# Kernel tuning notes

Measured on AMD Instinct MI355X. Metric: run time of the kernel, lower is better.

The kernel has to match this reference:

```python
import jax, jax.numpy as jnp
import numpy as np

B, T, V, E, H, L = 2, 1024, 50257, 768, 12, 12
D = E // H  # 64
FF = 4 * E
SCALE = 1.0 / (E * E)  # module divides scores by C**2 where C = embedding_dim
EPS = 1e-5


def _layernorm(x, g, b):
    m = jnp.mean(x, axis=-1, keepdims=True)
    v = jnp.mean((x - m) ** 2, axis=-1, keepdims=True)
    return (x - m) * jax.lax.rsqrt(v + EPS) * g + b


def setup_inputs() -> dict:
    key = jax.random.key(0)
    ks = jax.random.split(key, 12)
    s = 0.02
    f32 = jnp.float32
    return {
        "idx": jax.random.randint(ks[0], (B, T), 0, V),
        "tok_emb": jax.random.normal(ks[1], (V, E), f32) * s,
        "pos_emb": jax.random.normal(ks[2], (T, E), f32) * s,
        "Wk": jax.random.normal(ks[3], (L, H, E, D), f32) * s,
        "Wq": jax.random.normal(ks[4], (L, H, E, D), f32) * s,
        "Wv": jax.random.normal(ks[5], (L, H, E, D), f32) * s,
        "Wproj": jax.random.normal(ks[6], (L, E, E), f32) * s,
        "bproj": jnp.zeros((L, E), f32),
        "ln1_g": jnp.ones((L, E), f32),
        "ln1_b": jnp.zeros((L, E), f32),
        "W1": jax.random.normal(ks[7], (L, E, FF), f32) * s,
        "b1": jnp.zeros((L, FF), f32),
        "W2": jax.random.normal(ks[8], (L, FF, E), f32) * s,
        "b2": jnp.zeros((L, E), f32),
        "ln2_g": jnp.ones((L, E), f32),
        "ln2_b": jnp.zeros((L, E), f32),
        "lnf_g": jnp.ones((E,), f32),
        "lnf_b": jnp.zeros((E,), f32),
        "Wlm": jax.random.normal(ks[9], (E, V), f32) * s,
        "blm": jnp.zeros((V,), f32),
    }


def reference(idx, tok_emb, pos_emb, Wk, Wq, Wv, Wproj, bproj, ln1_g, ln1_b,
              W1, b1, W2, b2, ln2_g, ln2_b, lnf_g, lnf_b, Wlm, blm):
    x = tok_emb[idx] + pos_emb[:T]  # [B,T,E]
    causal = jnp.tril(jnp.ones((T, T), bool))

    def layer(x, p):
        wk, wq, wv, wp, bp, g1, be1, w1, bb1, w2, bb2, g2, be2 = p
        h = _layernorm(x, g1, be1)
        k = jnp.einsum('bte,hed->bhtd', h, wk)
        q = jnp.einsum('bte,hed->bhtd', h, wq)
        v = jnp.einsum('bte,hed->bhtd', h, wv)
        # faithful to source: scores = k @ q^T, scaled by 1/E^2
        scores = jnp.einsum('bhtd,bhsd->bhts', k, q) * SCALE
        scores = jnp.where(causal, scores, -jnp.inf)
        attn = jax.nn.softmax(scores, axis=-1)
        o = jnp.einsum('bhts,bhsd->bhtd', attn, v)
        o = o.transpose(0, 2, 1, 3).reshape(B, T, E)  # concat heads
        x = x + o @ wp + bp
        h2 = _layernorm(x, g2, be2)
        x = x + jax.nn.relu(h2 @ w1 + bb1) @ w2 + bb2
        return x, None

    x, _ = jax.lax.scan(layer, x, (Wk, Wq, Wv, Wproj, bproj, ln1_g, ln1_b,
                                   W1, b1, W2, b2, ln2_g, ln2_b))
    x = _layernorm(x, lnf_g, lnf_b)
    logits = x @ Wlm + blm  # [B,T,V]
    return logits
```

## Files before the change

### kernel.cpp

```cpp
#include <hip/hip_runtime.h>
#include <hip/hip_bf16.h>
#include <stdint.h>

#define B_    2
#define T_    1024
#define V_    50257
#define VPAD_ 50304
#define VPAD2_ 50432
#define E_    768
#define H_    12
#define L_    12
#define D_    64
#define FF_   3072
#define NTOK  (B_*T_)
#define SCALE_ (1.0f/((float)E_*(float)E_))

#define SWZ(r) ((((r) ^ ((r) >> 2)) & 3))

typedef float f32x4 __attribute__((ext_vector_type(4)));
typedef __bf16 bf16x8 __attribute__((ext_vector_type(8)));
typedef short short8 __attribute__((ext_vector_type(8)));

__device__ __forceinline__ float bits2f(short s) {
    unsigned u = ((unsigned)(unsigned short)s) << 16;
    float f; __builtin_memcpy(&f, &u, 4); return f;
}
__device__ __forceinline__ short f2b(float f) {
    unsigned u; __builtin_memcpy(&u, &f, 4);
    unsigned r = (u + 0x7FFFu + ((u >> 16) & 1u)) >> 16;
    return (short)r;
}

#define GLOAD16(gsrc, ldst) __builtin_amdgcn_global_load_lds( \
    (const __attribute__((address_space(1))) unsigned*)(gsrc), \
    (__attribute__((address_space(3))) unsigned*)(ldst), 16, 0, 0)

__global__ __launch_bounds__(256) void embed_kernel(
    const int* __restrict__ idx, const float* __restrict__ tok,
    const float* __restrict__ pos, float* __restrict__ x)
{
    int m = blockIdx.x, tid = threadIdx.x;
    int row = idx[m];
    int t = m & (T_-1);
    #pragma unroll
    for (int i = 0; i < 3; i++) {
        int e = tid + i*256;
        x[(size_t)m*E_ + e] = tok[(size_t)row*E_ + e] + pos[(size_t)t*E_ + e];
    }
}

__device__ __forceinline__ float block_sum256(float v, float* red) {
    #pragma unroll
    for (int off = 32; off; off >>= 1) v += __shfl_xor(v, off, 64);
    int w = threadIdx.x >> 6;
    __syncthreads();
    if ((threadIdx.x & 63) == 0) red[w] = v;
    __syncthreads();
    return red[0] + red[1] + red[2] + red[3];
}

__global__ __launch_bounds__(256) void ln_kernel(
    const float* __restrict__ x, const float* __restrict__ g,
    const float* __restrict__ bb, short* __restrict__ out)
{
    __shared__ float red[4];
    int m = blockIdx.x, tid = threadIdx.x;
    const float* xr = x + (size_t)m*E_;
    float loc[3]; float s = 0.f;
    #pragma unroll
    for (int i = 0; i < 3; i++) { loc[i] = xr[tid + i*256]; s += loc[i]; }
    s = block_sum256(s, red);
    float mean = s * (1.0f/E_);
    float vs = 0.f;
    #pragma unroll
    for (int i = 0; i < 3; i++) { float d = loc[i] - mean; vs += d*d; }
    vs = block_sum256(vs, red);
    float rstd = rsqrtf(vs * (1.0f/E_) + 1e-5f);
    #pragma unroll
    for (int i = 0; i < 3; i++) {
        int e = tid + i*256;
        out[(size_t)m*E_ + e] = f2b((loc[i] - mean) * rstd * g[e] + bb[e]);
    }
}

template<int NS>
__global__ __launch_bounds__(256) void ln_red(
    float* __restrict__ x, const float* __restrict__ pb,
    const float* __restrict__ bias,
    const float* __restrict__ g, const float* __restrict__ bb,
    short* __restrict__ out)
{
    __shared__ float red[4];
    int m = blockIdx.x, tid = threadIdx.x;
    float* xr = x + (size_t)m*E_;
    float loc[3]; float s = 0.f;
    #pragma unroll
    for (int i = 0; i < 3; i++) {
        int e = tid + i*256;
        float v = xr[e];
        if (NS > 0) {
            #pragma unroll
            for (int sp = 0; sp < NS; sp++)
                v += pb[((size_t)sp*NTOK + m)*E_ + e];
            v += bias[e];
            xr[e] = v;
        }
        loc[i] = v; s += v;
    }
    s = block_sum256(s, red);
    float mean = s * (1.0f/E_);
    float vs = 0.f;
    #pragma unroll
    for (int i = 0; i < 3; i++) { float d = loc[i] - mean; vs += d*d; }
    vs = block_sum256(vs, red);
    float rstd = rsqrtf(vs * (1.0f/E_) + 1e-5f);
    #pragma unroll
    for (int i = 0; i < 3; i++) {
        int e = tid + i*256;
        out[(size_t)m*E_ + e] = f2b((loc[i] - mean) * rstd * g[e] + bb[e]);
    }
}

__global__ __launch_bounds__(256) void pack_t(
    const float* __restrict__ src, short* __restrict__ dst,
    int srcK, int srcN, size_t sstride, size_t dstride)
{
    __shared__ float tile[64][65];
    int k0 = blockIdx.x*64, n0 = blockIdx.y*64, l = blockIdx.z;
    const float* s = src + (size_t)l*sstride;
    short* d = dst + (size_t)l*dstride;
    int tid = threadIdx.x;
    const bool vec = (srcN & 3) == 0;
    #pragma unroll
    for (int i = 0; i < 4; i++) {
        int r = (tid >> 4) + i*16;
        int c = (tid & 15) * 4;
        const float* sp = s + (size_t)(k0+r)*srcN + n0 + c;
        if (vec) {
            f32x4 v = *(const f32x4*)sp;
            tile[r][c+0] = v.x; tile[r][c+1] = v.y; tile[r][c+2] = v.z; tile[r][c+3] = v.w;
        } else {
            #pragma unroll
            for (int j = 0; j < 4; j++)
                tile[r][c+j] = (n0 + c + j < srcN) ? sp[j] : 0.f;
        }
    }
    __syncthreads();
    #pragma unroll
    for (int i = 0; i < 2; i++) {
        int r2  = (tid >> 3) + i*32;
        int grp = tid & 7;
        short8 o;
        #pragma unroll
        for (int j = 0; j < 8; j++) o[j] = f2b(tile[grp*8 + j][r2]);
        *(short8*)(d + (size_t)(n0+r2)*srcK + k0 + grp*8) = o;
    }
}

__global__ __launch_bounds__(256) void pack_qkv(
    const float* __restrict__ Wq, const float* __restrict__ Wk,
    const float* __restrict__ Wv, short* __restrict__ dst)
{
    __shared__ float tile[64][65];
    int e0 = blockIdx.x*64;
    int y = blockIdx.y, sel = y/12, h = y - sel*12;
    int l = blockIdx.z;
    const float* s = (sel == 0 ? Wq : (sel == 1 ? Wk : Wv)) + (((size_t)l*H_ + h)*E_)*D_;
    int tid = threadIdx.x;
    #pragma unroll
    for (int i = 0; i < 4; i++) {
        int r = (tid >> 4) + i*16;
        int c = (tid & 15) * 4;
        f32x4 v = *(const f32x4*)(s + (size_t)(e0+r)*D_ + c);
        tile[r][c+0] = v.x; tile[r][c+1] = v.y; tile[r][c+2] = v.z; tile[r][c+3] = v.w;
    }
    __syncthreads();
    short* d_ = dst + (size_t)l*2304*E_;
    #pragma unroll
    for (int i = 0; i < 2; i++) {
        int r2  = (tid >> 3) + i*32;
        int grp = tid & 7;
        short8 o;
        #pragma unroll
        for (int j = 0; j < 8; j++) o[j] = f2b(tile[grp*8 + j][r2]);
        *(short8*)(d_ + (size_t)(sel*768 + h*64 + r2)*E_ + e0 + grp*8) = o;
    }
}

template<int MODE>
__global__ __launch_bounds__(256) void gemm3(
    const short* __restrict__ A, const short* __restrict__ Bt,
    const float* __restrict__ bias,
    float* __restrict__ X, short* __restrict__ Out, float* __restrict__ OutF,
    int K, int lda, int ldc, int Nreal, int cpx)
{
    __shared__ __align__(16) short As[3][128*32];
    __shared__ __align__(16) short Bs[3][128*32];

    const int tid  = threadIdx.x;
    const int lane = tid & 63, wv = tid >> 6;
    const int wm = wv & 1, wn = wv >> 1;

    int bid = blockIdx.x;
    int g   = (bid & 7)*cpx + (bid >> 3);
    const int m0 = (g & 15) * 128;
    const int n0 = (g >> 4) * 128;

    f32x4 acc[4][4];
    #pragma unroll
    for (int i = 0; i < 4; i++)
        #pragma unroll
        for (int j = 0; j < 4; j++) acc[i][j] = (f32x4){0.f,0.f,0.f,0.f};

    const int srow0 = wv*32 + (lane >> 2);
    const int ssl   = lane & 3;

#define STAGE3(buf, kk) do {                                                  \
    _Pragma("unroll")                                                         \
    for (int i_ = 0; i_ < 2; i_++) {                                          \
        int row_ = srow0 + i_*16;                                             \
        int sl_  = ssl ^ SWZ(row_);                                           \
        GLOAD16(A  + (size_t)(m0 + row_)*lda + (kk) + sl_*8,                  \
                &As[buf][(wv*128 + i_*64)*8]);                                \
        GLOAD16(Bt + (size_t)(n0 + row_)*K   + (kk) + sl_*8,                  \
                &Bs[buf][(wv*128 + i_*64)*8]);                                \
    } } while(0)

    const int nt = K >> 5;
    STAGE3(0, 0);
    if (nt > 1) STAGE3(1, 32);

    int cur = 0, nxt2 = 2;
    for (int kt = 0; kt < nt; ++kt) {
        if (kt + 1 < nt) asm volatile("s_waitcnt vmcnt(4)" ::: "memory");
        else             asm volatile("s_waitcnt vmcnt(0)" ::: "memory");
        __builtin_amdgcn_s_barrier();

        bf16x8 af[4], bf[4];
        #pragma unroll
        for (int mi = 0; mi < 4; mi++) {
            int row = wm*64 + mi*16 + (lane & 15);
            af[mi] = *(const bf16x8*)&As[cur][row*32 + (((lane >> 4) ^ SWZ(row)))*8];
        }
        #pragma unroll
        for (int ni = 0; ni < 4; ni++) {
            int col = wn*64 + ni*16 + (lane & 15);
            bf[ni] = *(const bf16x8*)&Bs[cur][col*32 + (((lane >> 4) ^ SWZ(col)))*8];
        }
        if (kt + 2 < nt) STAGE3(nxt2, (kt + 2) << 5);

        #pragma unroll
        for (int ni = 0; ni < 4; ni++)
            #pragma unroll
            for (int mi = 0; mi < 4; mi++)
                acc[mi][ni] = __builtin_amdgcn_mfma_f32_16x16x32_bf16(af[mi], bf[ni], acc[mi][ni], 0,0,0);

        cur  = (cur  == 2) ? 0 : cur + 1;
        nxt2 = (nxt2 == 2) ? 0 : nxt2 + 1;
    }
#undef STAGE3

    const int rb = (lane >> 4) << 2;
    const int cb = lane & 15;
    #pragma unroll
    for (int mi = 0; mi < 4; mi++) {
      #pragma unroll
      for (int ni = 0; ni < 4; ni++) {
        #pragma unroll
        for (int j = 0; j < 4; j++) {
            int row = m0 + wm*64 + mi*16 + rb + j;
            int col = n0 + wn*64 + ni*16 + cb;
            float v = acc[mi][ni][j];
            if (MODE == 0) {
                if (col < Nreal) OutF[(size_t)row*ldc + col] = v + bias[col];
            } else if (MODE == 1) {
                v += bias[col];
                v = v > 0.f ? v : 0.f;
                Out[(size_t)row*ldc + col] = f2b(v);
            } else {
                int nsel = col / 768;
                int c = col - nsel*768;
                int h = c >> 6, d = c & 63;
                int b = row >> 10, t = row & (T_-1);
                short* dst = Out + (size_t)nsel*((size_t)NTOK*E_);
                dst[(((size_t)(b*H_ + h)*T_ + t) << 6) + d] = f2b(v);
            }
        }
      }
    }
}

__global__ __launch_bounds__(512) void gemm_lm(
    const short* __restrict__ A, const short* __restrict__ Bt,
    const float* __restrict__ bias, float* __restrict__ OutF,
    int K, int lda, int ldc, int Nreal, int cpx)
{
    __shared__ __align__(16) short As[3][256*32];
    __shared__ __align__(16) short Bs[3][256*32];

    const int tid  = threadIdx.x;
    const int lane = tid & 63, wv = tid >> 6;
    const int wm = wv & 1, wn = wv >> 1;

    int bid = blockIdx.x;
    int g   = (bid & 7)*cpx + (bid >> 3);
    const int m0 = (g & 7) * 256;
    const int n0 = (g >> 3) * 256;

    f32x4 acc[8][4];
    #pragma unroll
    for (int i = 0; i < 8; i++)
        #pragma unroll
        for (int j = 0; j < 4; j++) acc[i][j] = (f32x4){0.f,0.f,0.f,0.f};

    const int srow0 = wv*16 + (lane >> 2);
    const int ssl   = lane & 3;

#define STAGELM(buf, kk) do {                                                 \
    _Pragma("unroll")                                                         \
    for (int i_ = 0; i_ < 2; i_++) {                                          \
        int row_ = srow0 + i_*128;                                            \
        int sl_  = ssl ^ SWZ(row_);                                           \
        GLOAD16(A  + (size_t)(m0 + row_)*lda + (kk) + sl_*8,                  \
                &As[buf][(i_*512 + wv*64)*8]);                                \
        GLOAD16(Bt + (size_t)(n0 + row_)*K   + (kk) + sl_*8,                  \
                &Bs[buf][(i_*512 + wv*64)*8]);                                \
    } } while(0)

    const int nt = K >> 5;
    STAGELM(0, 0);
    if (nt > 1) STAGELM(1, 32);

    int cur = 0, nxt2 = 2;
    for (int kt = 0; kt < nt; ++kt) {
        if (kt + 1 < nt) asm volatile("s_waitcnt vmcnt(4)" ::: "memory");
        else             asm volatile("s_waitcnt vmcnt(0)" ::: "memory");
        __builtin_amdgcn_s_barrier();

        bf16x8 af[8], bf[4];
        #pragma unroll
        for (int mi = 0; mi < 8; mi++) {
            int row = wm*128 + mi*16 + (lane & 15);
            af[mi] = *(const bf16x8*)&As[cur][row*32 + (((lane >> 4) ^ SWZ(row)))*8];
        }
        #pragma unroll
        for (int ni = 0; ni < 4; ni++) {
            int col = wn*64 + ni*16 + (lane & 15);
            bf[ni] = *(const bf16x8*)&Bs[cur][col*32 + (((lane >> 4) ^ SWZ(col)))*8];
        }
        if (kt + 2 < nt) STAGELM(nxt2, (kt + 2) << 5);

        #pragma unroll
        for (int ni = 0; ni < 4; ni++)
            #pragma unroll
            for (int mi = 0; mi < 8; mi++)
                acc[mi][ni] = __builtin_amdgcn_mfma_f32_16x16x32_bf16(af[mi], bf[ni], acc[mi][ni], 0,0,0);

        cur  = (cur  == 2) ? 0 : cur + 1;
        nxt2 = (nxt2 == 2) ? 0 : nxt2 + 1;
    }
#undef STAGELM

    const int rb = (lane >> 4) << 2;
    const int cb = lane & 15;
    #pragma unroll
    for (int mi = 0; mi < 8; mi++) {
      #pragma unroll
      for (int ni = 0; ni < 4; ni++) {
        #pragma unroll
        for (int j = 0; j < 4; j++) {
            int row = m0 + wm*128 + mi*16 + rb + j;
            int col = n0 + wn*64 + ni*16 + cb;
            if (col < Nreal)
                OutF[(size_t)row*ldc + col] = acc[mi][ni][j] + bias[col];
        }
      }
    }
}

template<int SPLITS, bool ATOMIC>
__global__ __launch_bounds__(256) void gemm3_sk(
    const short* __restrict__ A, const short* __restrict__ Bt,
    const float* __restrict__ bias, float* __restrict__ X, float* __restrict__ PB,
    int K, int lda)
{
    __shared__ __align__(16) short As[3][128*32];
    __shared__ __align__(16) short Bs[3][128*32];

    const int tid  = threadIdx.x;
    const int lane = tid & 63, wv = tid >> 6;
    const int wm = wv & 1, wn = wv >> 1;

    const int panel = blockIdx.x / SPLITS;
    const int sp    = blockIdx.x % SPLITS;
    const int m0 = (panel & 15) * 128;
    const int n0 = (panel >> 4) * 128;
    const int Ks = K / SPLITS;
    const int kbeg = sp * Ks;

    f32x4 acc[4][4];
    #pragma unroll
    for (int i = 0; i < 4; i++)
        #pragma unroll
        for (int j = 0; j < 4; j++) acc[i][j] = (f32x4){0.f,0.f,0.f,0.f};

    const int srow0 = wv*32 + (lane >> 2);
    const int ssl   = lane & 3;

#define STAGESK(buf, kk) do {                                                 \
    _Pragma("unroll")                                                         \
    for (int i_ = 0; i_ < 2; i_++) {                                          \
        int row_ = srow0 + i_*16;                                             \
        int sl_  = ssl ^ SWZ(row_);                                           \
        GLOAD16(A  + (size_t)(m0 + row_)*lda + (kk) + sl_*8,                  \
                &As[buf][(wv*128 + i_*64)*8]);                                \
        GLOAD16(Bt + (size_t)(n0 + row_)*K   + (kk) + sl_*8,                  \
                &Bs[buf][(wv*128 + i_*64)*8]);                                \
    } } while(0)

    const int nt = Ks >> 5;
    STAGESK(0, kbeg);
    if (nt > 1) STAGESK(1, kbeg + 32);

    int cur = 0, nxt2 = 2;
    for (int kt = 0; kt < nt; ++kt) {
        if (kt + 1 < nt) asm volatile("s_waitcnt vmcnt(4)" ::: "memory");
        else             asm volatile("s_waitcnt vmcnt(0)" ::: "memory");
        __builtin_amdgcn_s_barrier();

        bf16x8 af[4], bf[4];
        #pragma unroll
        for (int mi = 0; mi < 4; mi++) {
            int row = wm*64 + mi*16 + (lane & 15);
            af[mi] = *(const bf16x8*)&As[cur][row*32 + (((lane >> 4) ^ SWZ(row)))*8];
        }
        #pragma unroll
        for (int ni = 0; ni < 4; ni++) {
            int col = wn*64 + ni*16 + (lane & 15);
            bf[ni] = *(const bf16x8*)&Bs[cur][col*32 + (((lane >> 4) ^ SWZ(col)))*8];
        }
        if (kt + 2 < nt) STAGESK(nxt2, kbeg + ((kt + 2) << 5));

        #pragma unroll
        for (int ni = 0; ni < 4; ni++)
            #pragma unroll
            for (int mi = 0; mi < 4; mi++)
                acc[mi][ni] = __builtin_amdgcn_mfma_f32_16x16x32_bf16(af[mi], bf[ni], acc[mi][ni], 0,0,0);

        cur  = (cur  == 2) ? 0 : cur + 1;
        nxt2 = (nxt2 == 2) ? 0 : nxt2 + 1;
    }
#undef STAGESK

    const int rb = (lane >> 4) << 2;
    const int cb = lane & 15;
    #pragma unroll
    for (int mi = 0; mi < 4; mi++) {
      #pragma unroll
      for (int ni = 0; ni < 4; ni++) {
        #pragma unroll
        for (int j = 0; j < 4; j++) {
            int row = m0 + wm*64 + mi*16 + rb + j;
            int col = n0 + wn*64 + ni*16 + cb;
            float v = acc[mi][ni][j];
            if (ATOMIC) {
                if (sp == 0) v += bias[col];
                atomicAdd(&X[(size_t)row*E_ + col], v);
            } else {
                PB[((size_t)sp*NTOK + row)*E_ + col] = v;
            }
        }
      }
    }
}

__global__ __launch_bounds__(256) void attn2(
    const short* __restrict__ qg, const short* __restrict__ kg,
    const short* __restrict__ vg, short* __restrict__ ao)
{
    __shared__ __align__(16) short Kt[64*64];
    __shared__ __align__(16) short Qs[64*64];
    __shared__ __align__(16) short Vs[64*64];
    __shared__ __align__(16) short Ps[4][16*64];

    const int tid = threadIdx.x, lane = tid & 63, w = tid >> 6, g = lane >> 4;
    const int t0 = blockIdx.x * 64;
    const int bh = blockIdx.y;
    const size_t base = (size_t)bh * T_ * 64;

    #pragma unroll
    for (int is = 0; is < 2; is++) {
        int idx = is*256 + tid;
        int row = idx >> 3, sl = idx & 7;
        short8 v = *(const short8*)(kg + base + (size_t)(t0+row)*64 + sl*8);
        *(short8*)&Kt[row*64 + (sl ^ (row&7))*8] = v;
    }
    __syncthreads();

    bf16x8 akt[2];
    {
        int lt = w*16 + (lane & 15);
        #pragma unroll
        for (int c = 0; c < 2; c++)
            akt[c] = *(const bf16x8*)&Kt[lt*64 + ((c*4+g) ^ (lt&7))*8];
    }

    f32x4 o[4]; float m_run[4], l_run[4];
    #pragma unroll
    for (int i = 0; i < 4; i++) { o[i] = (f32x4){0,0,0,0}; m_run[i] = -1e30f; l_run[i] = 0.f; }

    const int qrow = tid >> 3, qsl = tid & 7;
    const int vd0 = (tid & 31) * 2;
    const int vsh = tid >> 5;

    short8 qv[2];
    unsigned vvr[8];

#define REGLOAD(s0_) do {                                                        \
    _Pragma("unroll")                                                            \
    for (int is_ = 0; is_ < 2; is_++)                                            \
        qv[is_] = *(const short8*)(qg + base + (size_t)((s0_) + qrow + is_*32)*64 + qsl*8); \
    _Pragma("unroll")                                                            \
    for (int i_ = 0; i_ < 8; i_++)                                               \
        vvr[i_] = *(const unsigned*)(vg + base + (size_t)((s0_) + vsh*8 + i_)*64 + vd0);    \
    } while(0)

    const int ntiles = (t0 >> 6) + 1;
    REGLOAD(0);

    for (int it = 0; it < ntiles; ++it) {
        __syncthreads();
        #pragma unroll
        for (int is = 0; is < 2; is++) {
            int row = qrow + is*32;
            *(short8*)&Qs[row*64 + (qsl ^ (row&7))*8] = qv[is];
        }
        #pragma unroll
        for (int dp = 0; dp < 2; dp++) {
            int d = vd0 + dp;
            short tmp[8];
            #pragma unroll
            for (int i = 0; i < 8; i++) tmp[i] = (short)((vvr[i] >> (dp*16)) & 0xffffu);
            *(short8*)&Vs[d*64 + (vsh ^ (d&7))*8] = *(short8*)tmp;
        }
        if (it + 1 < ntiles) REGLOAD((it+1)*64);
        __syncthreads();

        const int s0 = it*64;
        f32x4 s4[4];
        #pragma unroll
        for (int j = 0; j < 4; j++) s4[j] = (f32x4){0,0,0,0};
        #pragma unroll
        for (int c = 0; c < 2; c++) {
            #pragma unroll
            for (int j = 0; j < 4; j++) {
                int sr = j*16 + (lane & 15);
                bf16x8 bq = *(const bf16x8*)&Qs[sr*64 + ((c*4+g) ^ (sr&7))*8];
                s4[j] = __builtin_amdgcn_mfma_f32_16x16x32_bf16(akt[c], bq, s4[j], 0,0,0);
            }
        }
        float p[4][4];
        const bool diag = (it == ntiles-1);
        #pragma unroll
        for (int j = 0; j < 4; j++) {
          #pragma unroll
          for (int r = 0; r < 4; r++) {
            float v = s4[j][r] * SCALE_;
            if (diag) {
                int tglob = t0 + w*16 + g*4 + r;
                int sglob = s0 + j*16 + (lane & 15);
                if (sglob > tglob) v = -1e30f;
            }
            p[j][r] = v;
          }
        }
        #pragma unroll
        for (int r = 0; r < 4; r++) {
            float mx = fmaxf(fmaxf(p[0][r], p[1][r]), fmaxf(p[2][r], p[3][r]));
            #pragma unroll
            for (int off = 1; off < 16; off <<= 1) mx = fmaxf(mx, __shfl_xor(mx, off, 64));
            float mnew  = fmaxf(m_run[r], mx);
            float alpha = __expf(m_run[r] - mnew);
            float rs = 0.f;
            #pragma unroll
            for (int j = 0; j < 4; j++) { p[j][r] = __expf(p[j][r] - mnew); rs += p[j][r]; }
            #pragma unroll
            for (int off = 1; off < 16; off <<= 1) rs += __shfl_xor(rs, off, 64);
            l_run[r] = l_run[r]*alpha + rs;
            m_run[r] = mnew;
            #pragma unroll
            for (int ni = 0; ni < 4; ni++) o[ni][r] *= alpha;
        }
        #pragma unroll
        for (int j = 0; j < 4; j++) {
          #pragma unroll
          for (int r = 0; r < 4; r++) {
            int tl = g*4 + r, sc = j*16 + (lane & 15);
            Ps[w][tl*64 + ((sc>>3) ^ (tl&7))*8 + (sc&7)] = f2b(p[j][r]);
          }
        }
        asm volatile("s_waitcnt lgkmcnt(0)" ::: "memory");
        __builtin_amdgcn_sched_barrier(0);
        #pragma unroll
        for (int c = 0; c < 2; c++) {
            int tl = lane & 15;
            bf16x8 pa = *(const bf16x8*)&Ps[w][tl*64 + ((c*4+g) ^ (tl&7))*8];
            #pragma unroll
            for (int ni = 0; ni < 4; ni++) {
                int d = ni*16 + (lane & 15);
                bf16x8 bv = *(const bf16x8*)&Vs[d*64 + ((c*4+g) ^ (d&7))*8];
                o[ni] = __builtin_amdgcn_mfma_f32_16x16x32_bf16(pa, bv, o[ni], 0,0,0);
            }
        }
    }
#undef REGLOAD

    const int b = bh / H_, h = bh - b*H_;
    #pragma unroll
    for (int ni = 0; ni < 4; ni++) {
      #pragma unroll
      for (int r = 0; r < 4; r++) {
        int t = t0 + w*16 + g*4 + r;
        int d = ni*16 + (lane & 15);
        ao[((size_t)(b*T_ + t))*E_ + h*64 + d] = f2b(o[ni][r] / l_run[r]);
      }
    }
}

template<int MODE, bool QKV3>
__global__ __launch_bounds__(256) void gemm2(
    const short* __restrict__ A,
    const float* __restrict__ Bq, const float* __restrict__ Bk2, const float* __restrict__ Bv2,
    const float* __restrict__ bias,
    float* __restrict__ X, short* __restrict__ Out, float* __restrict__ OutF,
    int M, int Ntot, int K, int lda, int kstride, int ldc)
{
    __shared__ __align__(16) short As[128*32];
    __shared__ __align__(16) short Bs[128*32];

    const int tid  = threadIdx.x;
    const int lane = tid & 63, wave = tid >> 6;
    const int wm = wave & 1, wn = wave >> 1;
    const int m0 = blockIdx.x * 128;
    const int n0 = blockIdx.y * 128;
    const int g  = lane >> 4;

    const float* Bm = Bq;
    int nsel = 0, c0 = n0;
    if (QKV3) {
        nsel = n0 / 768;
        c0 = n0 - nsel*768;
        Bm = (nsel == 0) ? Bq : (nsel == 1 ? Bk2 : Bv2);
    }

    f32x4 acc[4][4];
    #pragma unroll
    for (int i = 0; i < 4; i++)
        #pragma unroll
        for (int j = 0; j < 4; j++) acc[i][j] = (f32x4){0.f,0.f,0.f,0.f};

    const int bn  = tid & 127;
    const int bkh = tid >> 7;
    const int cg  = c0 + bn;
    const bool bvalid = QKV3 ? true : (cg < Ntot);
    size_t bbase;
    if (QKV3) bbase = (size_t)(cg >> 6) * ((size_t)E_*D_) + (cg & 63);
    else      bbase = (size_t)cg;

    for (int k0 = 0; k0 < K; k0 += 32) {
        #pragma unroll
        for (int is = 0; is < 2; is++) {
            int idx = is*256 + tid;
            int row = idx >> 2, sl = idx & 3;
            short8 v = *(const short8*)(A + (size_t)(m0+row)*lda + k0 + sl*8);
            int sl2 = sl ^ ((row ^ (row>>2)) & 3);
            *(short8*)&As[row*32 + sl2*8] = v;
        }
        {
            float bv[16];
            #pragma unroll
            for (int i = 0; i < 16; i++) {
                int k = k0 + bkh*16 + i;
                bv[i] = bvalid ? Bm[bbase + (size_t)k*kstride] : 0.f;
            }
            short bh16[16];
            #pragma unroll
            for (int i = 0; i < 16; i++) {
                __bf16 h = (__bf16)bv[i];
                bh16[i] = __builtin_bit_cast(short, h);
            }
            #pragma unroll
            for (int q = 0; q < 2; q++) {
                int kb  = bkh*2 + q;
                int sl2 = kb ^ ((bn ^ (bn>>2)) & 3);
                *(short8*)&Bs[bn*32 + sl2*8] = *(short8*)&bh16[q*8];
            }
        }
        __syncthreads();

        bf16x8 af[4];
        #pragma unroll
        for (int mi = 0; mi < 4; mi++) {
            int row = wm*64 + mi*16 + (lane & 15);
            int sl2 = g ^ ((row ^ (row>>2)) & 3);
            af[mi] = *(const bf16x8*)&As[row*32 + sl2*8];
        }
        #pragma unroll
        for (int ni = 0; ni < 4; ni++) {
            int nn  = wn*64 + ni*16 + (lane & 15);
            int sl2 = g ^ ((nn ^ (nn>>2)) & 3);
            bf16x8 bfr = *(const bf16x8*)&Bs[nn*32 + sl2*8];
            #pragma unroll
            for (int mi = 0; mi < 4; mi++)
                acc[mi][ni] = __builtin_amdgcn_mfma_f32_16x16x32_bf16(af[mi], bfr, acc[mi][ni], 0,0,0);
        }
        __syncthreads();
    }

    const int rb = g << 2;
    const int cb = lane & 15;
    #pragma unroll
    for (int mi = 0; mi < 4; mi++) {
      #pragma unroll
      for (int ni = 0; ni < 4; ni++) {
        #pragma unroll
        for (int j = 0; j < 4; j++) {
            int row = m0 + wm*64 + mi*16 + rb + j;
            int col = n0 + wn*64 + ni*16 + cb;
            float v = acc[mi][ni][j];
            if (MODE == 0) {
                if (col < Ntot) OutF[(size_t)row*ldc + col] = v + bias[col];
            } else if (MODE == 1) {
                v += bias[col];
                v = v > 0.f ? v : 0.f;
                Out[(size_t)row*ldc + col] = f2b(v);
            } else if (MODE == 2) {
                X[(size_t)row*E_ + col] += v + bias[col];
            } else {
                int c = col - nsel*768;
                int h = c >> 6, d = c & 63;
                int b = row >> 10, t = row & (T_-1);
                short* dst = Out + (size_t)nsel*((size_t)NTOK*E_);
                dst[(((size_t)(b*H_ + h)*T_ + t) << 6) + d] = f2b(v);
            }
        }
      }
    }
}

extern "C" void kernel_launch(void* const* d_in, const int* in_sizes, int n_in,
                              void* d_out, int out_size, void* d_ws, size_t ws_size,
                              hipStream_t stream)
{
    (void)in_sizes; (void)n_in; (void)out_size;

    const int*   idx     = (const int*)  d_in[0];
    const float* tok_emb = (const float*)d_in[1];
    const float* pos_emb = (const float*)d_in[2];
    const float* Wk      = (const float*)d_in[3];
    const float* Wq      = (const float*)d_in[4];
    const float* Wv      = (const float*)d_in[5];
    const float* Wproj   = (const float*)d_in[6];
    const float* bproj   = (const float*)d_in[7];
    const float* ln1_g   = (const float*)d_in[8];
    const float* ln1_b   = (const float*)d_in[9];
    const float* W1      = (const float*)d_in[10];
    const float* b1      = (const float*)d_in[11];
    const float* W2      = (const float*)d_in[12];
    const float* b2      = (const float*)d_in[13];
    const float* ln2_g   = (const float*)d_in[14];
    const float* ln2_b   = (const float*)d_in[15];
    const float* lnf_g   = (const float*)d_in[16];
    const float* lnf_b   = (const float*)d_in[17];
    const float* Wlm     = (const float*)d_in[18];
    const float* blm     = (const float*)d_in[19];
    float* out = (float*)d_out;

    char* w = (char*)d_ws;
    float* x    = (float*)w; w += (size_t)NTOK*E_*4;
    short* hbuf = (short*)w; w += (size_t)NTOK*E_*2;
    short* qb   = (short*)w; w += (size_t)NTOK*E_*2;
    short* kb   = (short*)w; w += (size_t)NTOK*E_*2;
    short* vb   = (short*)w; w += (size_t)NTOK*E_*2;
    short* aob  = (short*)w; w += (size_t)NTOK*E_*2;
    short* midb = (short*)w; w += (size_t)NTOK*FF_*2;
    float* pbuf = (float*)w; w += (size_t)4*NTOK*E_*4;

    const size_t act_bytes = (size_t)(w - (char*)d_ws);
    const size_t wqkv_n = (size_t)L_*2304*E_;
    const size_t wproj_n = (size_t)L_*E_*E_;
    const size_t wff_n = (size_t)L_*E_*FF_;
    const size_t wlm_n = (size_t)VPAD2_*E_;
    const size_t need = act_bytes + 2*(wqkv_n + wproj_n + 2*wff_n + wlm_n);

    const size_t HED = (size_t)H_*E_*D_;
    dim3 gAT(T_/64, B_*H_);

    embed_kernel<<<NTOK, 256, 0, stream>>>(idx, tok_emb, pos_emb, x);

    if (ws_size >= need) {
        short* qkvw = (short*)w; w += wqkv_n*2;
        short* projw= (short*)w; w += wproj_n*2;
        short* w1w  = (short*)w; w += wff_n*2;
        short* w2w  = (short*)w; w += wff_n*2;
        short* lmw  = (short*)w;

        pack_qkv<<<dim3(E_/64, 36, L_), 256, 0, stream>>>(Wq, Wk, Wv, qkvw);
        pack_t<<<dim3(E_/64, E_/64, L_), 256, 0, stream>>>(Wproj, projw, E_, E_, (size_t)E_*E_, (size_t)E_*E_);
        pack_t<<<dim3(E_/64, FF_/64, L_), 256, 0, stream>>>(W1, w1w, E_, FF_, (size_t)E_*FF_, (size_t)E_*FF_);
        pack_t<<<dim3(FF_/64, E_/64, L_), 256, 0, stream>>>(W2, w2w, FF_, E_, (size_t)E_*FF_, (size_t)E_*FF_);
        pack_t<<<dim3(E_/64, VPAD2_/64, 1), 256, 0, stream>>>(Wlm, lmw, E_, V_, 0, 0);

        const int nQKV = 16*(2304/128), nF1 = 16*(FF_/128);
        const int nP = 16*(E_/128);
        const int nLM2 = 8*(VPAD2_/256);

        for (int l = 0; l < L_; l++) {
            if (l == 0)
                ln_red<0><<<NTOK, 256, 0, stream>>>(x, nullptr, nullptr,
                    ln1_g + (size_t)l*E_, ln1_b + (size_t)l*E_, hbuf);
            else
                ln_red<4><<<NTOK, 256, 0, stream>>>(x, pbuf, b2 + (size_t)(l-1)*E_,
                    ln1_g + (size_t)l*E_, ln1_b + (size_t)l*E_, hbuf);

            gemm3<3><<<nQKV, 256, 0, stream>>>(hbuf, qkvw + (size_t)l*2304*E_, nullptr,
                                               nullptr, qb, nullptr, E_, E_, 0, 2304, nQKV/8);
            attn2<<<gAT, 256, 0, stream>>>(qb, kb, vb, aob);

            gemm3_sk<2,false><<<nP*2, 256, 0, stream>>>(aob, projw + (size_t)l*E_*E_,
                                                        nullptr, nullptr, pbuf, E_, E_);
            ln_red<2><<<NTOK, 256, 0, stream>>>(x, pbuf, bproj + (size_t)l*E_,
                ln2_g + (size_t)l*E_, ln2_b + (size_t)l*E_, hbuf);

            gemm3<1><<<nF1, 256, 0, stream>>>(hbuf, w1w + (size_t)l*E_*FF_, b1 + (size_t)l*FF_,
                                              nullptr, midb, nullptr, E_, E_, FF_, FF_, nF1/8);
            gemm3_sk<4,false><<<nP*4, 256, 0, stream>>>(midb, w2w + (size_t)l*E_*FF_,
                                                        nullptr, nullptr, pbuf, FF_, FF_);
        }
        ln_red<4><<<NTOK, 256, 0, stream>>>(x, pbuf, b2 + (size_t)(L_-1)*E_, lnf_g, lnf_b, hbuf);
        gemm_lm<<<nLM2, 512, 0, stream>>>(hbuf, lmw, blm, out, E_, E_, V_, V_, nLM2/8);
    } else {
        dim3 gQKV(16, 18), gP(16, 6), gF1(16, 24), gLM(16, 393);
        for (int l = 0; l < L_; l++) {
            ln_kernel<<<NTOK, 256, 0, stream>>>(x, ln1_g + (size_t)l*E_, ln1_b + (size_t)l*E_, hbuf);
            gemm2<3,true><<<gQKV, 256, 0, stream>>>(hbuf,
                Wq + (size_t)l*HED, Wk + (size_t)l*HED, Wv + (size_t)l*HED,
                nullptr, nullptr, qb, nullptr, NTOK, 2304, E_, E_, 64, 0);
            attn2<<<gAT, 256, 0, stream>>>(qb, kb, vb, aob);
            gemm2<2,false><<<gP, 256, 0, stream>>>(aob,
                Wproj + (size_t)l*E_*E_, nullptr, nullptr, bproj + (size_t)l*E_,
                x, nullptr, nullptr, NTOK, E_, E_, E_, E_, 0);
            ln_kernel<<<NTOK, 256, 0, stream>>>(x, ln2_g + (size_t)l*E_, ln2_b + (size_t)l*E_, hbuf);
            gemm2<1,false><<<gF1, 256, 0, stream>>>(hbuf,
                W1 + (size_t)l*E_*FF_, nullptr, nullptr, b1 + (size_t)l*FF_,
                nullptr, midb, nullptr, NTOK, FF_, E_, E_, FF_, FF_);
            gemm2<2,false><<<gP, 256, 0, stream>>>(midb,
                W2 + (size_t)l*FF_*E_, nullptr, nullptr, b2 + (size_t)l*E_,
                x, nullptr, nullptr, NTOK, E_, FF_, FF_, E_, 0);
        }
        ln_kernel<<<NTOK, 256, 0, stream>>>(x, lnf_g, lnf_b, hbuf);
        gemm2<0,false><<<gLM, 256, 0, stream>>>(hbuf,
            Wlm, nullptr, nullptr, blm,
            nullptr, nullptr, out, NTOK, V_, E_, E_, V_, V_);
    }
}
```

Measured before the change: 1.921 ms.

## Restructure LM-head GEMM into ping-pong double-buffered BK=64 pipeline with setprio

```diff
diff --git a/kernel.cpp b/kernel.cpp
--- a/kernel.cpp
+++ b/kernel.cpp
@@ -5,7 +5,6 @@
 #define B_    2
 #define T_    1024
 #define V_    50257
-#define VPAD_ 50304
 #define VPAD2_ 50432
 #define E_    768
 #define H_    12
@@ -290,17 +289,18 @@
     }
 }
 
-__global__ __launch_bounds__(512) void gemm_lm(
+__global__ __launch_bounds__(512, 2) void gemm_lm(
     const short* __restrict__ A, const short* __restrict__ Bt,
     const float* __restrict__ bias, float* __restrict__ OutF,
     int K, int lda, int ldc, int Nreal, int cpx)
 {
-    __shared__ __align__(16) short As[3][256*32];
-    __shared__ __align__(16) short Bs[3][256*32];
+    __shared__ __align__(16) short As[2][2][128*64];
+    __shared__ __align__(16) short Bs[2][2][128*64];
 
     const int tid  = threadIdx.x;
     const int lane = tid & 63, wv = tid >> 6;
     const int wm = wv & 1, wn = wv >> 1;
+    const int bh = wn >> 1;
 
     int bid = blockIdx.x;
     int g   = (bid & 7)*cpx + (bid >> 3);
@@ -313,53 +313,79 @@
         #pragma unroll
         for (int j = 0; j < 4; j++) acc[i][j] = (f32x4){0.f,0.f,0.f,0.f};
 
-    const int srow0 = wv*16 + (lane >> 2);
-    const int ssl   = lane & 3;
-
-#define STAGELM(buf, kk) do {                                                 \
+#define STAGE_ALL(buf, kt) do {                                               \
     _Pragma("unroll")                                                         \
-    for (int i_ = 0; i_ < 2; i_++) {                                          \
-        int row_ = srow0 + i_*128;                                            \
-        int sl_  = ssl ^ SWZ(row_);                                           \
-        GLOAD16(A  + (size_t)(m0 + row_)*lda + (kk) + sl_*8,                  \
-                &As[buf][(i_*512 + wv*64)*8]);                                \
-        GLOAD16(Bt + (size_t)(n0 + row_)*K   + (kk) + sl_*8,                  \
-                &Bs[buf][(i_*512 + wv*64)*8]);                                \
+    for (int r_ = 0; r_ < 2; r_++) {                                          \
+        int c_  = r_*512 + wv*64 + lane;                                      \
+        int row_ = c_ >> 3;                                                   \
+        int ls_  = (c_ & 7) ^ (row_ & 7);                                     \
+        GLOAD16(A  + (size_t)(m0 +       row_)*lda + (kt)*64 + ls_*8, &As[buf][0][c_*8]); \
+        GLOAD16(A  + (size_t)(m0 + 128 + row_)*lda + (kt)*64 + ls_*8, &As[buf][1][c_*8]); \
+        GLOAD16(Bt + (size_t)(n0 +       row_)*K   + (kt)*64 + ls_*8, &Bs[buf][0][c_*8]); \
+        GLOAD16(Bt + (size_t)(n0 + 128 + row_)*K   + (kt)*64 + ls_*8, &Bs[buf][1][c_*8]); \
     } } while(0)
 
-    const int nt = K >> 5;
-    STAGELM(0, 0);
-    if (nt > 1) STAGELM(1, 32);
-
-    int cur = 0, nxt2 = 2;
+    bf16x8 afr[8], bfr[2];
+
+#define READ_A(ks) do {                                                       \
+    _Pragma("unroll")                                                         \
+    for (int mi = 0; mi < 8; mi++) {                                          \
+        int row = mi*16 + (lane & 15);                                        \
+        int sl  = ((ks)*4 + (lane >> 4)) ^ (row & 7);                         \
+        afr[mi] = *(const bf16x8*)&As[cur][wm][row*64 + sl*8];                \
+    } } while(0)
+
+#define READ_B2(nbase, ks) do {                                               \
+    _Pragma("unroll")                                                         \
+    for (int q = 0; q < 2; q++) {                                             \
+        int col = (wn & 1)*64 + ((nbase)+q)*16 + (lane & 15);                 \
+        int sl  = ((ks)*4 + (lane >> 4)) ^ (col & 7);                         \
+        bfr[q] = *(const bf16x8*)&Bs[cur][bh][col*64 + sl*8];                 \
+    } } while(0)
+
+#define MFMA16(nbase) do {                                                    \
+    __builtin_amdgcn_s_setprio(1);                                            \
+    _Pragma("unroll")                                                         \
+    for (int q = 0; q < 2; q++)                                               \
+        _Pragma("unroll")                                                     \
+        for (int mi = 0; mi < 8; mi++)                                        \
+            acc[mi][(nbase)+q] = __builtin_amdgcn_mfma_f32_16x16x32_bf16(     \
+                afr[mi], bfr[q], acc[mi][(nbase)+q], 0,0,0);                  \
+    __builtin_amdgcn_s_setprio(0);                                            \
+    } while(0)
+
+    const int nt = K >> 6;
+    STAGE_ALL(0, 0);
+    asm volatile("s_waitcnt vmcnt(0)" ::: "memory");
+    __builtin_amdgcn_s_barrier();
+
+    int cur = 0;
     for (int kt = 0; kt < nt; ++kt) {
-        if (kt + 1 < nt) asm volatile("s_waitcnt vmcnt(4)" ::: "memory");
-        else             asm volatile("s_waitcnt vmcnt(0)" ::: "memory");
-        __builtin_amdgcn_s_barrier();
-
-        bf16x8 af[8], bf[4];
-        #pragma unroll
-        for (int mi = 0; mi < 8; mi++) {
-            int row = wm*128 + mi*16 + (lane & 15);
-            af[mi] = *(const bf16x8*)&As[cur][row*32 + (((lane >> 4) ^ SWZ(row)))*8];
-        }
-        #pragma unroll
-        for (int ni = 0; ni < 4; ni++) {
-            int col = wn*64 + ni*16 + (lane & 15);
-            bf[ni] = *(const bf16x8*)&Bs[cur][col*32 + (((lane >> 4) ^ SWZ(col)))*8];
-        }
-        if (kt + 2 < nt) STAGELM(nxt2, (kt + 2) << 5);
-
-        #pragma unroll
-        for (int ni = 0; ni < 4; ni++)
-            #pragma unroll
-            for (int mi = 0; mi < 8; mi++)
-                acc[mi][ni] = __builtin_amdgcn_mfma_f32_16x16x32_bf16(af[mi], bf[ni], acc[mi][ni], 0,0,0);
-
-        cur  = (cur  == 2) ? 0 : cur + 1;
-        nxt2 = (nxt2 == 2) ? 0 : nxt2 + 1;
-    }
-#undef STAGELM
+        const int nb = cur ^ 1;
+        if (kt + 1 < nt) STAGE_ALL(nb, kt + 1);
+        READ_A(0); READ_B2(0, 0);
+        __builtin_amdgcn_s_barrier();
+        MFMA16(0);
+        __builtin_amdgcn_s_barrier();
+        READ_B2(2, 0);
+        __builtin_amdgcn_s_barrier();
+        MFMA16(2);
+        __builtin_amdgcn_s_barrier();
+        READ_A(1); READ_B2(0, 1);
+        __builtin_amdgcn_s_barrier();
+        MFMA16(0);
+        __builtin_amdgcn_s_barrier();
+        READ_B2(2, 1);
+        __builtin_amdgcn_s_barrier();
+        MFMA16(2);
+        if (kt + 1 < nt) asm volatile("s_waitcnt vmcnt(0)" ::: "memory");
+        __builtin_amdgcn_s_barrier();
+        cur = nb;
+    }
+#undef STAGE_ALL
+#undef READ_A
+#undef READ_B2
+#undef MFMA16
 
     const int rb = (lane >> 4) << 2;
     const int cb = lane & 15;
```

Result: slower. 1.976 ms (+2.9%).
